# Performance work log

Measured on AMD Instinct MI355X. Metric: run time of the kernel, lower is better.

Reference implementation:

```python
import jax, jax.numpy as jnp
import numpy as np

N = 100000
E = 1_600_000
DIN = 24
DH = 64
DOUT = 12
NEG_SLOPE = 0.01  # torch F.leaky_relu default


def setup_inputs() -> dict:
    key = jax.random.key(0)
    ks = jax.random.split(key, 18)
    inp = {}
    inp["feats"] = jax.random.normal(ks[0], (N, DIN), dtype=jnp.float32)
    inp["e_w"] = jax.random.uniform(ks[1], (E, 1), dtype=jnp.float32)
    inp["snorm_n"] = jnp.ones((N, 1), dtype=jnp.float32)
    inp["snorm_e"] = jnp.ones((E, 1), dtype=jnp.float32)
    inp["src"] = jax.random.randint(ks[2], (E,), 0, N, dtype=jnp.int32)
    inp["dst"] = jax.random.randint(ks[3], (E,), 0, N, dtype=jnp.int32)
    s = 0.05
    inp["emb_h_W"] = jax.random.normal(ks[4], (DH, DIN), dtype=jnp.float32) * s
    inp["emb_h_b"] = jnp.zeros((DH,), dtype=jnp.float32)
    inp["emb_e_W"] = jax.random.normal(ks[5], (DH, 1), dtype=jnp.float32) * s
    inp["emb_e_b"] = jnp.zeros((DH,), dtype=jnp.float32)
    inp["W_self1"] = jax.random.normal(ks[6], (DH, DH), dtype=jnp.float32) * s
    inp["W_func1"] = jax.random.normal(ks[7], (DH, DH), dtype=jnp.float32) * s
    inp["attn1"] = jax.random.normal(ks[8], (3 * DH,), dtype=jnp.float32) * s
    inp["W_self2"] = jax.random.normal(ks[9], (DH, DH), dtype=jnp.float32) * s
    inp["W_func2"] = jax.random.normal(ks[10], (DH, DH), dtype=jnp.float32) * s
    inp["attn2"] = jax.random.normal(ks[11], (3 * DH,), dtype=jnp.float32) * s
    inp["lin1_W"] = jax.random.normal(ks[12], (DOUT, DH), dtype=jnp.float32) * s
    inp["lin1_b"] = jnp.zeros((DOUT,), dtype=jnp.float32)
    return inp


def _gat_layer(h, w_edge, src, dst, W_self, W_func, attn):
    # h: [N, d], w_edge: [E, d] edge embedding, attn: [3d]
    h_s = h @ W_self.T                       # linear_self(h)
    z = h @ W_func.T                         # linear_func(h)
    d = z.shape[-1]
    a_src, a_dst, a_w = attn[:d], attn[d:2 * d], attn[2 * d:]
    # attention score: W_a . [z_src, z_dst, w]  (decomposed to avoid [E,3d] concat)
    s_node_src = z @ a_src                   # [N]
    s_node_dst = z @ a_dst                   # [N]
    e = s_node_src[src] + s_node_dst[dst] + w_edge @ a_w  # [E]
    e = jax.nn.leaky_relu(e, NEG_SLOPE)
    # segment softmax over incoming edges per destination node
    m = jax.ops.segment_max(e, dst, num_segments=h.shape[0])
    ex = jnp.exp(e - m[dst])
    denom = jax.ops.segment_sum(ex, dst, num_segments=h.shape[0])
    alpha = ex / denom[dst]                  # [E]
    msg = alpha[:, None] * z[src]            # [E, d]
    agg = jax.ops.segment_sum(msg, dst, num_segments=h.shape[0])  # [N, d]
    # DGL: nodes with no incoming edges keep their old 'h' (not h_s + agg)
    in_deg = jax.ops.segment_sum(jnp.ones_like(e), dst, num_segments=h.shape[0])
    h_mid = jnp.where((in_deg > 0)[:, None], h_s + agg, h)
    return h + jax.nn.relu(h_mid)            # relu then residual


def reference(feats, e_w, snorm_n, snorm_e, src, dst,
              emb_h_W, emb_h_b, emb_e_W, emb_e_b,
              W_self1, W_func1, attn1, W_self2, W_func2, attn2,
              lin1_W, lin1_b):
    feats = feats.reshape(feats.shape[0], -1)
    h = feats @ emb_h_W.T + emb_h_b          # [N, DH]
    e = e_w @ emb_e_W.T + emb_e_b            # [E, DH]
    h = _gat_layer(h, e, src, dst, W_self1, W_func1, attn1)
    h = _gat_layer(h, e, src, dst, W_self2, W_func2, attn2)
    y = h @ lin1_W.T + lin1_b                # [N, DOUT]
    return y
```

## Files before the change

kernel.cpp:

```cpp
#include <hip/hip_runtime.h>
#include <hip/hip_fp16.h>

#define N_NODES 100000
#define N_EDGES 1600000
#define DIN 24
#define DH 64
#define DOUT 12
#define NEG_SLOPE 0.01f
#define NG 64
#define EPG (N_EDGES / NG)
#define NS 4
#define SLICE_N 32768
#define NTOT (NG * N_NODES)
#define SCAN_BLK 4096
#define LDSW 72

#define NB_HIST (NS * NG)
#define NB_SUMDEG ((N_NODES + 255) / 256)
#define NB_SCAN1N ((N_NODES + SCAN_BLK - 1) / SCAN_BLK)
#define NB_SCAT4 ((N_EDGES / 4 + 1023) / 1024)
#define NB_NODE ((N_NODES + 63) / 64)
#define NB_NODE_T ((NB_NODE + 1) / 2)
#define NB_NME ((NB_NODE + 7) / 8)
#define NB_AGG ((N_NODES + 7) / 8)

#define SM_WEMB 18432
#define SM_BIAS 23552
#define SM_HBUF 23808
#define SM_SIZE 60672

typedef _Float16 half8_t __attribute__((ext_vector_type(8)));
typedef float floatx4 __attribute__((ext_vector_type(4)));

__device__ __forceinline__ void dev_consts(const float* emb_e_W, const float* emb_e_b,
                                           const float* attn1, const float* attn2,
                                           float* consts) {
    int lane = threadIdx.x;
    if (lane >= 64) return;
    float w = emb_e_W[lane], b = emb_e_b[lane];
    float a1 = attn1[2 * DH + lane], a2 = attn2[2 * DH + lane];
    float c11 = w * a1, c01 = b * a1, c12 = w * a2, c02 = b * a2;
    for (int off = 32; off; off >>= 1) {
        c11 += __shfl_down(c11, off);
        c01 += __shfl_down(c01, off);
        c12 += __shfl_down(c12, off);
        c02 += __shfl_down(c02, off);
    }
    if (lane == 0) {
        consts[0] = c11; consts[1] = c01; consts[2] = c12; consts[3] = c02;
    }
}

__device__ __forceinline__ void dev_hist(int bid, char* smem, const int* dst,
                                         unsigned char* deg, unsigned char* rank) {
    unsigned* cnt = (unsigned*)smem;
    int s = bid % NS, c = bid / NS;
    for (int i = threadIdx.x; i < SLICE_N / 4; i += 1024) cnt[i] = 0;
    __syncthreads();
    int nbase = s * SLICE_N;
    int start = c * EPG, end = start + EPG;
    for (int i = start + threadIdx.x; i < end; i += 1024) {
        int local = dst[i] - nbase;
        if ((unsigned)local < SLICE_N) {
            unsigned sh = (unsigned)(local & 3) * 8u;
            unsigned old = atomicAdd(&cnt[local >> 2], 1u << sh);
            rank[i] = (unsigned char)((old >> sh) & 255u);
        }
    }
    __syncthreads();
    int nmax = N_NODES - nbase;
    if (nmax > SLICE_N) nmax = SLICE_N;
    unsigned* dw = (unsigned*)(deg + (size_t)c * N_NODES + nbase);
    for (int l = threadIdx.x; l < (nmax >> 2); l += 1024) dw[l] = cnt[l];
}

__device__ __forceinline__ void dev_scan1(int bid, const int* in, int* out,
                                          int* part, int n) {
    __shared__ int lds[256];
    int t = threadIdx.x;
    int base = bid * SCAN_BLK + t * 16;
    int v[16];
    int s = 0;
#pragma unroll
    for (int i = 0; i < 16; ++i) {
        int idx = base + i;
        v[i] = (idx < n) ? in[idx] : 0;
        s += v[i];
    }
    lds[t] = s;
    __syncthreads();
    for (int off = 1; off < 256; off <<= 1) {
        int y = (t >= off) ? lds[t - off] : 0;
        __syncthreads();
        lds[t] += y;
        __syncthreads();
    }
    int run = lds[t] - s;
#pragma unroll
    for (int i = 0; i < 16; ++i) {
        int idx = base + i;
        if (idx < n) out[idx] = run;
        run += v[i];
    }
    if (t == 255) part[bid] = lds[255];
}

__device__ __forceinline__ void dev_sumdeg(int bid, const unsigned char* degB,
                                           int* degN, unsigned char* chunkOff) {
    int n = bid * 256 + threadIdx.x;
    if (n >= N_NODES) return;
    int run = 0;
    for (int g = 0; g < NG; ++g) {
        size_t idx = (size_t)g * N_NODES + n;
        int v = (int)degB[idx];
        chunkOff[idx] = (unsigned char)run;
        run += v;
    }
    degN[n] = run;
}

__device__ __forceinline__ void dev_scat4(int bid, const int* src, const int* dst,
                                          const float* e_w, const unsigned char* rank,
                                          const int* rowStart,
                                          const unsigned char* chunkOff,
                                          unsigned* csr2) {
    int e4 = (bid * 1024 + threadIdx.x) * 4;
    if (e4 >= N_EDGES) return;
    int g = e4 / EPG;
    const unsigned char* co = chunkOff + (size_t)g * N_NODES;
    int4   d4 = *(const int4*)(dst + e4);
    int4   s4 = *(const int4*)(src + e4);
    float4 w4 = *(const float4*)(e_w + e4);
    unsigned r4 = *(const unsigned*)(rank + e4);
    int b0 = rowStart[d4.x] + (int)co[d4.x];
    int b1 = rowStart[d4.y] + (int)co[d4.y];
    int b2 = rowStart[d4.z] + (int)co[d4.z];
    int b3 = rowStart[d4.w] + (int)co[d4.w];
    unsigned q0 = (unsigned)(w4.x * 32768.f); if (q0 > 32767u) q0 = 32767u;
    unsigned q1 = (unsigned)(w4.y * 32768.f); if (q1 > 32767u) q1 = 32767u;
    unsigned q2 = (unsigned)(w4.z * 32768.f); if (q2 > 32767u) q2 = 32767u;
    unsigned q3 = (unsigned)(w4.w * 32768.f); if (q3 > 32767u) q3 = 32767u;
    csr2[b0 + (r4 & 255u)]         = (unsigned)s4.x | (q0 << 17);
    csr2[b1 + ((r4 >> 8) & 255u)]  = (unsigned)s4.y | (q1 << 17);
    csr2[b2 + ((r4 >> 16) & 255u)] = (unsigned)s4.z | (q2 << 17);
    csr2[b3 + (r4 >> 24)]          = (unsigned)s4.w | (q3 << 17);
}

__device__ __forceinline__ void dev_nodeME(int bid, char* smem,
                                           const float* feats, const float* embW,
                                           const float* embB,
                                           const float* Wself, const float* Wfunc,
                                           const float* attn,
                                           __half* h16, __half* zh, __half* hs16,
                                           float* s_src, float* s_dst) {
    _Float16* lds   = (_Float16*)smem;
    _Float16* wembH = (_Float16*)(smem + SM_WEMB);
    float*    biasS = (float*)(smem + SM_BIAS);
    _Float16* hbufA = (_Float16*)(smem + SM_HBUF);
    int tid = threadIdx.x;
    for (int idx = tid; idx < 2 * 64 * 64; idx += 1024) {
        int mat = idx >> 12, rem = idx & 4095;
        int o = rem >> 6, k = rem & 63;
        float v = mat ? Wfunc[rem] : Wself[rem];
        lds[(mat * 64 + o) * LDSW + k] = (_Float16)v;
    }
    for (int idx = tid; idx < 64 * 32; idx += 1024) {
        int o = idx >> 5, k = idx & 31;
        wembH[o * 40 + k] = (_Float16)((k < DIN) ? embW[o * DIN + k] : 0.f);
    }
    if (tid < 64) biasS[tid] = embB[tid];
    __syncthreads();

    int wave = tid >> 6, lane = tid & 63;
    int vb = wave >> 2, wv = wave & 3;
    int quad = lane >> 4, lm = lane & 15;
    float asv[4], adv[4];
#pragma unroll
    for (int t = 0; t < 4; ++t) {
        asv[t] = attn[t * 16 + lm];
        adv[t] = attn[DH + t * 16 + lm];
    }
    const _Float16* bS = lds;
    const _Float16* bF = lds + 64 * LDSW;
    _Float16* hb = hbufA + wave * (16 * 72);

    for (int tb = bid * 4 + vb; tb < NB_NODE; tb += NB_NME * 4) {
        int n0 = (tb * 4 + wv) * 16;
        if (n0 >= N_NODES) continue;

        half8_t afE;
#pragma unroll
        for (int j = 0; j < 8; ++j) afE[j] = (_Float16)0.f;
        if (quad < 3) {
            const float* f = feats + (size_t)(n0 + lm) * DIN + quad * 8;
            float4 q0 = *(const float4*)(f);
            float4 q1 = *(const float4*)(f + 4);
            afE[0] = (_Float16)q0.x; afE[1] = (_Float16)q0.y;
            afE[2] = (_Float16)q0.z; afE[3] = (_Float16)q0.w;
            afE[4] = (_Float16)q1.x; afE[5] = (_Float16)q1.y;
            afE[6] = (_Float16)q1.z; afE[7] = (_Float16)q1.w;
        }
        floatx4 accE[4];
#pragma unroll
        for (int t = 0; t < 4; ++t) accE[t] = (floatx4)0.f;
#pragma unroll
        for (int t = 0; t < 4; ++t) {
            int o = t * 16 + lm;
            half8_t bE = *(const half8_t*)(wembH + o * 40 + quad * 8);
            accE[t] = __builtin_amdgcn_mfma_f32_16x16x32_f16(afE, bE, accE[t], 0, 0, 0);
        }
#pragma unroll
        for (int t = 0; t < 4; ++t) {
            float bv = biasS[t * 16 + lm];
#pragma unroll
            for (int r = 0; r < 4; ++r) {
                float hv = accE[t][r] + bv;
                int node = n0 + quad * 4 + r;
                h16[(size_t)node * DH + t * 16 + lm] = __float2half(hv);
                hb[(quad * 4 + r) * 72 + t * 16 + lm] = (_Float16)hv;
            }
        }
        half8_t afrag[2];
#pragma unroll
        for (int ks = 0; ks < 2; ++ks)
            afrag[ks] = *(const half8_t*)(hb + lm * 72 + ks * 32 + quad * 8);

        floatx4 accS[4], accF[4];
#pragma unroll
        for (int t = 0; t < 4; ++t) { accS[t] = (floatx4)0.f; accF[t] = (floatx4)0.f; }
#pragma unroll
        for (int t = 0; t < 4; ++t) {
            int o = t * 16 + lm;
#pragma unroll
            for (int ks = 0; ks < 2; ++ks) {
                int hoff = o * LDSW + ks * 32 + quad * 8;
                half8_t b1 = *(const half8_t*)(bS + hoff);
                half8_t b2 = *(const half8_t*)(bF + hoff);
                accS[t] = __builtin_amdgcn_mfma_f32_16x16x32_f16(afrag[ks], b1, accS[t], 0, 0, 0);
                accF[t] = __builtin_amdgcn_mfma_f32_16x16x32_f16(afrag[ks], b2, accF[t], 0, 0, 0);
            }
        }

        float ps[4] = {0.f, 0.f, 0.f, 0.f}, pd[4] = {0.f, 0.f, 0.f, 0.f};
#pragma unroll
        for (int t = 0; t < 4; ++t) {
#pragma unroll
            for (int r = 0; r < 4; ++r) {
                int node = n0 + quad * 4 + r;
                float zv = accF[t][r];
                zh[(size_t)node * DH + t * 16 + lm] = __float2half(zv);
                hs16[(size_t)node * DH + t * 16 + lm] = __float2half(accS[t][r]);
                ps[r] += zv * asv[t];
                pd[r] += zv * adv[t];
            }
        }
#pragma unroll
        for (int r = 0; r < 4; ++r) {
            float p1 = ps[r], p2 = pd[r];
            for (int off = 8; off; off >>= 1) {
                p1 += __shfl_xor(p1, off);
                p2 += __shfl_xor(p2, off);
            }
            if (lm == 0) {
                s_src[n0 + quad * 4 + r] = p1;
                s_dst[n0 + quad * 4 + r] = p2;
            }
        }
    }
}

__device__ __forceinline__ void dev_nodeM(int bid, int stride, const __half* h16,
                                          const float* Wself, const float* Wfunc,
                                          const float* attn,
                                          __half* zh, __half* hs16,
                                          float* s_src, float* s_dst) {
    __shared__ _Float16 lds[2 * 64 * LDSW];
    int tid = threadIdx.x;
    for (int idx = tid; idx < 2 * 64 * 64; idx += 256) {
        int mat = idx >> 12, rem = idx & 4095;
        int o = rem >> 6, k = rem & 63;
        float v = mat ? Wfunc[rem] : Wself[rem];
        lds[(mat * 64 + o) * LDSW + k] = (_Float16)v;
    }
    __syncthreads();

    int wave = tid >> 6, lane = tid & 63;
    int quad = lane >> 4, lm = lane & 15;
    float asv[4], adv[4];
#pragma unroll
    for (int t = 0; t < 4; ++t) {
        asv[t] = attn[t * 16 + lm];
        adv[t] = attn[DH + t * 16 + lm];
    }
    const _Float16* bS = lds;
    const _Float16* bF = lds + 64 * LDSW;

    for (int tb = bid; tb < NB_NODE; tb += stride) {
        int n0 = (tb * 4 + wave) * 16;
        if (n0 >= N_NODES) continue;

        const _Float16* hrow = (const _Float16*)h16 + (size_t)(n0 + lm) * DH;
        half8_t afrag[2];
#pragma unroll
        for (int ks = 0; ks < 2; ++ks)
            afrag[ks] = *(const half8_t*)(hrow + ks * 32 + quad * 8);

        floatx4 accS[4], accF[4];
#pragma unroll
        for (int t = 0; t < 4; ++t) { accS[t] = (floatx4)0.f; accF[t] = (floatx4)0.f; }

#pragma unroll
        for (int t = 0; t < 4; ++t) {
            int o = t * 16 + lm;
#pragma unroll
            for (int ks = 0; ks < 2; ++ks) {
                int hoff = o * LDSW + ks * 32 + quad * 8;
                half8_t b1 = *(const half8_t*)(bS + hoff);
                half8_t b2 = *(const half8_t*)(bF + hoff);
                accS[t] = __builtin_amdgcn_mfma_f32_16x16x32_f16(afrag[ks], b1, accS[t], 0, 0, 0);
                accF[t] = __builtin_amdgcn_mfma_f32_16x16x32_f16(afrag[ks], b2, accF[t], 0, 0, 0);
            }
        }

        float ps[4] = {0.f, 0.f, 0.f, 0.f}, pd[4] = {0.f, 0.f, 0.f, 0.f};
#pragma unroll
        for (int t = 0; t < 4; ++t) {
#pragma unroll
            for (int r = 0; r < 4; ++r) {
                int node = n0 + quad * 4 + r;
                float zv = accF[t][r];
                zh[(size_t)node * DH + t * 16 + lm] = __float2half(zv);
                hs16[(size_t)node * DH + t * 16 + lm] = __float2half(accS[t][r]);
                ps[r] += zv * asv[t];
                pd[r] += zv * adv[t];
            }
        }
#pragma unroll
        for (int r = 0; r < 4; ++r) {
            float p1 = ps[r], p2 = pd[r];
            for (int off = 8; off; off >>= 1) {
                p1 += __shfl_xor(p1, off);
                p2 += __shfl_xor(p2, off);
            }
            if (lm == 0) {
                s_src[n0 + quad * 4 + r] = p1;
                s_dst[n0 + quad * 4 + r] = p2;
            }
        }
    }
}

__global__ void __launch_bounds__(1024, 2)
k_fuse1(const int* __restrict__ dst, unsigned char* __restrict__ deg,
        unsigned char* __restrict__ rank,
        const float* __restrict__ emb_e_W, const float* __restrict__ emb_e_b,
        const float* __restrict__ attn1, const float* __restrict__ attn2,
        float* __restrict__ consts) {
    __shared__ __align__(16) char smem[SLICE_N];
    int bid = blockIdx.x;
    if (bid == 0) { dev_consts(emb_e_W, emb_e_b, attn1, attn2, consts); return; }
    dev_hist(bid - 1, smem, dst, deg, rank);
}

__global__ void k_prep2(const unsigned char* __restrict__ degB, int* __restrict__ degN,
                        unsigned char* __restrict__ chunkOff) {
    dev_sumdeg(blockIdx.x, degB, degN, chunkOff);
}

__global__ void k_prep3(const int* __restrict__ degN, int* __restrict__ row_offN,
                        int* __restrict__ partN) {
    dev_scan1(blockIdx.x, degN, row_offN, partN, N_NODES);
}

__global__ void k_prep4(const int* __restrict__ row_offN, const int* __restrict__ partN,
                        int* __restrict__ rowStart) {
    __shared__ int pfx[32];
    int t = threadIdx.x;
    if (t < 64) {
        int v = (t < NB_SCAN1N) ? partN[t] : 0;
        int x = v;
#pragma unroll
        for (int s = 1; s < 32; s <<= 1) {
            int y = __shfl_up(x, s);
            if (t >= s) x += y;
        }
        if (t < 32) pfx[t] = x - v;
    }
    __syncthreads();
    int n = blockIdx.x * 256 + t;
    if (n < N_NODES) rowStart[n] = row_offN[n] + pfx[n >> 12];
    if (n == 0) rowStart[N_NODES] = N_EDGES;
}

__global__ void __launch_bounds__(1024, 2)
k_fuse5(const float* __restrict__ feats, const float* __restrict__ embW,
        const float* __restrict__ embB,
        __half* __restrict__ h16, const float* __restrict__ Wself1,
        const float* __restrict__ Wfunc1, const float* __restrict__ attn1,
        __half* __restrict__ zh, __half* __restrict__ hs16,
        float* __restrict__ s_src, float* __restrict__ s_dst,
        const int* __restrict__ src, const int* __restrict__ dst,
        const float* __restrict__ e_w, const unsigned char* __restrict__ rank,
        const int* __restrict__ rowStart,
        const unsigned char* __restrict__ chunkOff, unsigned* __restrict__ csr2) {
    __shared__ __align__(16) char smem[SM_SIZE];
    int bid = blockIdx.x;
    if (bid < NB_NME) {
        dev_nodeME(bid, smem, feats, embW, embB, Wself1, Wfunc1, attn1,
                   h16, zh, hs16, s_src, s_dst);
        return;
    }
    dev_scat4(bid - NB_NME, src, dst, e_w, rank, rowStart, chunkOff, csr2);
}

__global__ void __launch_bounds__(256, 4)
k_nodeL(const __half* __restrict__ h16, const float* __restrict__ Wself,
        const float* __restrict__ Wfunc, const float* __restrict__ attn,
        __half* __restrict__ zh, __half* __restrict__ hs16,
        float* __restrict__ s_src, float* __restrict__ s_dst) {
    dev_nodeM(blockIdx.x, NB_NODE_T, h16, Wself, Wfunc, attn, zh, hs16, s_src, s_dst);
}

__global__ void k_agg(const int* __restrict__ rowStart,
                      const unsigned* __restrict__ csr,
                      const float* __restrict__ s_src, const float* __restrict__ s_dstA,
                      const float* __restrict__ consts, int layer,
                      const __half* __restrict__ zh, const __half* __restrict__ hsb,
                      __half* __restrict__ h16,
                      const float* __restrict__ lin_W, const float* __restrict__ lin_b,
                      float* __restrict__ y, int final_layer) {
    int wave = threadIdx.x >> 6, lane = threadIdx.x & 63;
    int half = lane >> 5, hl = lane & 31;
    int eg = (lane >> 3) & 3, c8 = lane & 7;
    int n = blockIdx.x * 8 + wave * 2 + half;
    if (n >= N_NODES) return;
    int rs = rowStart[n];
    int deg = rowStart[n + 1] - rs;
    int degO = __shfl_xor(deg, 32);
    int degmax = deg > degO ? deg : degO;

    float c1 = consts[layer * 2 + 0];
    float c0 = consts[layer * 2 + 1];
    float sd = s_dstA[n];

    float acc[8];
#pragma unroll
    for (int k = 0; k < 8; ++k) acc[k] = 0.f;
    float ssl = 0.f;
    int lbase = lane & 32;

    for (int base = 0; base < degmax; base += 32) {
        float ex = 0.f;
        int s0 = 0;
        int idx = base + hl;
        if (idx < deg) {
            unsigned w = csr[rs + idx];
            s0 = (int)(w & 0x1FFFFu);
            float ew = (float)(w >> 17) * (1.f / 32768.f);
            float e = s_src[s0] + sd + ew * c1 + c0;
            e = (e > 0.f) ? e : NEG_SLOPE * e;
            ex = __expf(e);
        }
        ssl += ex;
        int cnt = degmax - base;
        if (cnt > 32) cnt = 32;
#pragma unroll 4
        for (int jb = 0; jb < cnt; jb += 4) {
            int srcl = lbase + jb + eg;
            int sj = __shfl(s0, srcl);
            float exj = __shfl(ex, srcl);
            unsigned boff = ((unsigned)sj << 7) | ((unsigned)c8 << 4);
            half8_t zv = *(const half8_t*)((const char*)zh + boff);
#pragma unroll
            for (int k = 0; k < 8; ++k) acc[k] += exj * (float)zv[k];
        }
    }
#pragma unroll
    for (int k = 0; k < 8; ++k) {
        acc[k] += __shfl_xor(acc[k], 8);
        acc[k] += __shfl_xor(acc[k], 16);
    }
    ssl += __shfl_xor(ssl, 16); ssl += __shfl_xor(ssl, 8);
    ssl += __shfl_xor(ssl, 4);  ssl += __shfl_xor(ssl, 2);
    ssl += __shfl_xor(ssl, 1);

    unsigned noff = ((unsigned)n << 7) | ((unsigned)c8 << 4);
    half8_t hv8 = *(const half8_t*)((const char*)h16 + noff);
    float hold[8];
#pragma unroll
    for (int k = 0; k < 8; ++k) hold[k] = (float)hv8[k];
    float hnew[8];
    if (deg == 0) {
#pragma unroll
        for (int k = 0; k < 8; ++k) hnew[k] = hold[k] + fmaxf(hold[k], 0.f);
    } else {
        float rinv = 1.f / ssl;
        half8_t hs8 = *(const half8_t*)((const char*)hsb + noff);
#pragma unroll
        for (int k = 0; k < 8; ++k)
            hnew[k] = hold[k] + fmaxf((float)hs8[k] + acc[k] * rinv, 0.f);
    }

    if (!final_layer) {
        if (eg == 0) {
            half8_t o8;
#pragma unroll
            for (int k = 0; k < 8; ++k) o8[k] = (_Float16)hnew[k];
            *(half8_t*)((char*)h16 + noff) = o8;
        }
    } else {
#pragma unroll
        for (int t = 0; t < 3; ++t) {
            int o = eg * 3 + t;
            const float* wr = lin_W + o * DH + c8 * 8;
            float p = 0.f;
#pragma unroll
            for (int k = 0; k < 8; ++k) p += hnew[k] * wr[k];
            p += __shfl_xor(p, 1); p += __shfl_xor(p, 2); p += __shfl_xor(p, 4);
            if (c8 == 0) y[n * DOUT + o] = p + lin_b[o];
        }
    }
}

extern "C" void kernel_launch(void* const* d_in, const int* in_sizes, int n_in,
                              void* d_out, int out_size, void* d_ws, size_t ws_size,
                              hipStream_t stream) {
    const float* feats   = (const float*)d_in[0];
    const float* e_w     = (const float*)d_in[1];
    const int*   src     = (const int*)d_in[4];
    const int*   dst     = (const int*)d_in[5];
    const float* emb_h_W = (const float*)d_in[6];
    const float* emb_h_b = (const float*)d_in[7];
    const float* emb_e_W = (const float*)d_in[8];
    const float* emb_e_b = (const float*)d_in[9];
    const float* Wself[2] = {(const float*)d_in[10], (const float*)d_in[13]};
    const float* Wfunc[2] = {(const float*)d_in[11], (const float*)d_in[14]};
    const float* attn[2]  = {(const float*)d_in[12], (const float*)d_in[15]};
    const float* lin1_W  = (const float*)d_in[16];
    const float* lin1_b  = (const float*)d_in[17];
    float* y = (float*)d_out;

    char* ws = (char*)d_ws;
    size_t off = 0;
    auto alloc = [&](size_t bytes) {
        void* p = ws + off;
        off += (bytes + 255) & ~(size_t)255;
        return p;
    };
    __half*         h16      = (__half*)alloc((size_t)N_NODES * DH * 2);
    __half*         zh       = (__half*)alloc((size_t)N_NODES * DH * 2);
    __half*         hs16     = (__half*)alloc((size_t)N_NODES * DH * 2);
    unsigned*       csr2     = (unsigned*)alloc((size_t)N_EDGES * 4);
    float*          s_src    = (float*)alloc((size_t)N_NODES * 4);
    float*          s_dst    = (float*)alloc((size_t)N_NODES * 4);
    int*            row_offN = (int*)alloc((size_t)(N_NODES + 1) * 4);
    int*            rowStart = (int*)alloc((size_t)(N_NODES + 1) * 4);
    unsigned char*  deg      = (unsigned char*)alloc((size_t)NTOT + 256);
    unsigned char*  chunkOff = (unsigned char*)alloc((size_t)NTOT + 256);
    unsigned char*  rank     = (unsigned char*)alloc((size_t)N_EDGES);
    int*            degN     = (int*)alloc((size_t)N_NODES * 4);
    int*            partN    = (int*)alloc(1024 * 4);
    float*          consts   = (float*)alloc(4 * 4);

    k_fuse1<<<1 + NB_HIST, 1024, 0, stream>>>(dst, deg, rank, emb_e_W, emb_e_b,
                                              attn[0], attn[1], consts);
    k_prep2<<<NB_SUMDEG, 256, 0, stream>>>(deg, degN, chunkOff);
    k_prep3<<<NB_SCAN1N, 256, 0, stream>>>(degN, row_offN, partN);
    k_prep4<<<NB_SUMDEG, 256, 0, stream>>>(row_offN, partN, rowStart);
    k_fuse5<<<NB_NME + NB_SCAT4, 1024, 0, stream>>>(
        feats, emb_h_W, emb_h_b, h16, Wself[0], Wfunc[0], attn[0],
        zh, hs16, s_src, s_dst,
        src, dst, e_w, rank, rowStart, chunkOff, csr2);
    k_agg<<<NB_AGG, 256, 0, stream>>>(rowStart, csr2, s_src, s_dst, consts, 0,
                                      zh, hs16, h16, lin1_W, lin1_b, y, 0);
    k_nodeL<<<NB_NODE_T, 256, 0, stream>>>(h16, Wself[1], Wfunc[1], attn[1],
                                           zh, hs16, s_src, s_dst);
    k_agg<<<NB_AGG, 256, 0, stream>>>(rowStart, csr2, s_src, s_dst, consts, 1,
                                      zh, hs16, h16, lin1_W, lin1_b, y, 1);
}
```

Baseline: 286.7 us.

## Fuse layer-1 aggregation with layer-2 node transform into one kernel

```diff
diff --git a/kernel.cpp b/kernel.cpp
--- a/kernel.cpp
+++ b/kernel.cpp
@@ -20,8 +20,8 @@
 #define NB_SCAN1N ((N_NODES + SCAN_BLK - 1) / SCAN_BLK)
 #define NB_SCAT4 ((N_EDGES / 4 + 1023) / 1024)
 #define NB_NODE ((N_NODES + 63) / 64)
-#define NB_NODE_T ((NB_NODE + 1) / 2)
 #define NB_NME ((NB_NODE + 7) / 8)
+#define NB_AGGG (N_NODES / 16)
 #define NB_AGG ((N_NODES + 7) / 8)
 
 #define SM_WEMB 18432
@@ -269,87 +269,6 @@
     }
 }
 
-__device__ __forceinline__ void dev_nodeM(int bid, int stride, const __half* h16,
-                                          const float* Wself, const float* Wfunc,
-                                          const float* attn,
-                                          __half* zh, __half* hs16,
-                                          float* s_src, float* s_dst) {
-    __shared__ _Float16 lds[2 * 64 * LDSW];
-    int tid = threadIdx.x;
-    for (int idx = tid; idx < 2 * 64 * 64; idx += 256) {
-        int mat = idx >> 12, rem = idx & 4095;
-        int o = rem >> 6, k = rem & 63;
-        float v = mat ? Wfunc[rem] : Wself[rem];
-        lds[(mat * 64 + o) * LDSW + k] = (_Float16)v;
-    }
-    __syncthreads();
-
-    int wave = tid >> 6, lane = tid & 63;
-    int quad = lane >> 4, lm = lane & 15;
-    float asv[4], adv[4];
-#pragma unroll
-    for (int t = 0; t < 4; ++t) {
-        asv[t] = attn[t * 16 + lm];
-        adv[t] = attn[DH + t * 16 + lm];
-    }
-    const _Float16* bS = lds;
-    const _Float16* bF = lds + 64 * LDSW;
-
-    for (int tb = bid; tb < NB_NODE; tb += stride) {
-        int n0 = (tb * 4 + wave) * 16;
-        if (n0 >= N_NODES) continue;
-
-        const _Float16* hrow = (const _Float16*)h16 + (size_t)(n0 + lm) * DH;
-        half8_t afrag[2];
-#pragma unroll
-        for (int ks = 0; ks < 2; ++ks)
-            afrag[ks] = *(const half8_t*)(hrow + ks * 32 + quad * 8);
-
-        floatx4 accS[4], accF[4];
-#pragma unroll
-        for (int t = 0; t < 4; ++t) { accS[t] = (floatx4)0.f; accF[t] = (floatx4)0.f; }
-
-#pragma unroll
-        for (int t = 0; t < 4; ++t) {
-            int o = t * 16 + lm;
-#pragma unroll
-            for (int ks = 0; ks < 2; ++ks) {
-                int hoff = o * LDSW + ks * 32 + quad * 8;
-                half8_t b1 = *(const half8_t*)(bS + hoff);
-                half8_t b2 = *(const half8_t*)(bF + hoff);
-                accS[t] = __builtin_amdgcn_mfma_f32_16x16x32_f16(afrag[ks], b1, accS[t], 0, 0, 0);
-                accF[t] = __builtin_amdgcn_mfma_f32_16x16x32_f16(afrag[ks], b2, accF[t], 0, 0, 0);
-            }
-        }
-
-        float ps[4] = {0.f, 0.f, 0.f, 0.f}, pd[4] = {0.f, 0.f, 0.f, 0.f};
-#pragma unroll
-        for (int t = 0; t < 4; ++t) {
-#pragma unroll
-            for (int r = 0; r < 4; ++r) {
-                int node = n0 + quad * 4 + r;
-                float zv = accF[t][r];
-                zh[(size_t)node * DH + t * 16 + lm] = __float2half(zv);
-                hs16[(size_t)node * DH + t * 16 + lm] = __float2half(accS[t][r]);
-                ps[r] += zv * asv[t];
-                pd[r] += zv * adv[t];
-            }
-        }
-#pragma unroll
-        for (int r = 0; r < 4; ++r) {
-            float p1 = ps[r], p2 = pd[r];
-            for (int off = 8; off; off >>= 1) {
-                p1 += __shfl_xor(p1, off);
-                p2 += __shfl_xor(p2, off);
-            }
-            if (lm == 0) {
-                s_src[n0 + quad * 4 + r] = p1;
-                s_dst[n0 + quad * 4 + r] = p2;
-            }
-        }
-    }
-}
-
 __global__ void __launch_bounds__(1024, 2)
 k_fuse1(const int* __restrict__ dst, unsigned char* __restrict__ deg,
         unsigned char* __restrict__ rank,
@@ -413,12 +332,164 @@
     dev_scat4(bid - NB_NME, src, dst, e_w, rank, rowStart, chunkOff, csr2);
 }
 
-__global__ void __launch_bounds__(256, 4)
-k_nodeL(const __half* __restrict__ h16, const float* __restrict__ Wself,
-        const float* __restrict__ Wfunc, const float* __restrict__ attn,
-        __half* __restrict__ zh, __half* __restrict__ hs16,
-        float* __restrict__ s_src, float* __restrict__ s_dst) {
-    dev_nodeM(blockIdx.x, NB_NODE_T, h16, Wself, Wfunc, attn, zh, hs16, s_src, s_dst);
+__global__ void __launch_bounds__(512, 6)
+k_aggG(const int* __restrict__ rowStart, const unsigned* __restrict__ csr,
+       const float* __restrict__ s_src, const float* __restrict__ s_dstA,
+       const float* __restrict__ consts,
+       const __half* __restrict__ zh, const __half* __restrict__ hsb,
+       __half* __restrict__ h16,
+       const float* __restrict__ Wself, const float* __restrict__ Wfunc,
+       const float* __restrict__ attn,
+       __half* __restrict__ zh2, __half* __restrict__ hs2,
+       float* __restrict__ s_src2, float* __restrict__ s_dst2) {
+    __shared__ _Float16 wlds[2 * 64 * LDSW];
+    __shared__ _Float16 hbuf[16 * 72];
+    int tid = threadIdx.x;
+    for (int idx = tid; idx < 2 * 64 * 64; idx += 512) {
+        int mat = idx >> 12, rem = idx & 4095;
+        int o = rem >> 6, k = rem & 63;
+        float v = mat ? Wfunc[rem] : Wself[rem];
+        wlds[(mat * 64 + o) * LDSW + k] = (_Float16)v;
+    }
+
+    int wave = tid >> 6, lane = tid & 63;
+    int half = lane >> 5, hl = lane & 31;
+    int eg = (lane >> 3) & 3, c8 = lane & 7;
+    int n = blockIdx.x * 16 + wave * 2 + half;
+    int rs = rowStart[n];
+    int deg = rowStart[n + 1] - rs;
+    int degO = __shfl_xor(deg, 32);
+    int degmax = deg > degO ? deg : degO;
+
+    float c1 = consts[0];
+    float c0 = consts[1];
+    float sd = s_dstA[n];
+
+    float acc[8];
+#pragma unroll
+    for (int k = 0; k < 8; ++k) acc[k] = 0.f;
+    float ssl = 0.f;
+    int lbase = lane & 32;
+
+    for (int base = 0; base < degmax; base += 32) {
+        float ex = 0.f;
+        int s0 = 0;
+        int idx = base + hl;
+        if (idx < deg) {
+            unsigned w = csr[rs + idx];
+            s0 = (int)(w & 0x1FFFFu);
+            float ew = (float)(w >> 17) * (1.f / 32768.f);
+            float e = s_src[s0] + sd + ew * c1 + c0;
+            e = (e > 0.f) ? e : NEG_SLOPE * e;
+            ex = __expf(e);
+        }
+        ssl += ex;
+        int cnt = degmax - base;
+        if (cnt > 32) cnt = 32;
+#pragma unroll 4
+        for (int jb = 0; jb < cnt; jb += 4) {
+            int srcl = lbase + jb + eg;
+            int sj = __shfl(s0, srcl);
+            float exj = __shfl(ex, srcl);
+            unsigned boff = ((unsigned)sj << 7) | ((unsigned)c8 << 4);
+            half8_t zv = *(const half8_t*)((const char*)zh + boff);
+#pragma unroll
+            for (int k = 0; k < 8; ++k) acc[k] += exj * (float)zv[k];
+        }
+    }
+#pragma unroll
+    for (int k = 0; k < 8; ++k) {
+        acc[k] += __shfl_xor(acc[k], 8);
+        acc[k] += __shfl_xor(acc[k], 16);
+    }
+    ssl += __shfl_xor(ssl, 16); ssl += __shfl_xor(ssl, 8);
+    ssl += __shfl_xor(ssl, 4);  ssl += __shfl_xor(ssl, 2);
+    ssl += __shfl_xor(ssl, 1);
+
+    unsigned noff = ((unsigned)n << 7) | ((unsigned)c8 << 4);
+    half8_t hv8 = *(const half8_t*)((const char*)h16 + noff);
+    float hold[8];
+#pragma unroll
+    for (int k = 0; k < 8; ++k) hold[k] = (float)hv8[k];
+    float hnew[8];
+    if (deg == 0) {
+#pragma unroll
+        for (int k = 0; k < 8; ++k) hnew[k] = hold[k] + fmaxf(hold[k], 0.f);
+    } else {
+        float rinv = 1.f / ssl;
+        half8_t hs8 = *(const half8_t*)((const char*)hsb + noff);
+#pragma unroll
+        for (int k = 0; k < 8; ++k)
+            hnew[k] = hold[k] + fmaxf((float)hs8[k] + acc[k] * rinv, 0.f);
+    }
+
+    if (eg == 0) {
+        half8_t o8;
+#pragma unroll
+        for (int k = 0; k < 8; ++k) o8[k] = (_Float16)hnew[k];
+        *(half8_t*)((char*)h16 + noff) = o8;
+        *(half8_t*)(hbuf + (wave * 2 + half) * 72 + c8 * 8) = o8;
+    }
+    __syncthreads();
+
+    if (wave == 0) {
+        int quad = lane >> 4, lm = lane & 15;
+        float asv[4], adv[4];
+#pragma unroll
+        for (int t = 0; t < 4; ++t) {
+            asv[t] = attn[t * 16 + lm];
+            adv[t] = attn[DH + t * 16 + lm];
+        }
+        half8_t afrag[2];
+#pragma unroll
+        for (int ks = 0; ks < 2; ++ks)
+            afrag[ks] = *(const half8_t*)(hbuf + lm * 72 + ks * 32 + quad * 8);
+
+        floatx4 accS[4], accF[4];
+#pragma unroll
+        for (int t = 0; t < 4; ++t) { accS[t] = (floatx4)0.f; accF[t] = (floatx4)0.f; }
+        const _Float16* bS = wlds;
+        const _Float16* bF = wlds + 64 * LDSW;
+#pragma unroll
+        for (int t = 0; t < 4; ++t) {
+            int o = t * 16 + lm;
+#pragma unroll
+            for (int ks = 0; ks < 2; ++ks) {
+                int hoff = o * LDSW + ks * 32 + quad * 8;
+                half8_t b1 = *(const half8_t*)(bS + hoff);
+                half8_t b2 = *(const half8_t*)(bF + hoff);
+                accS[t] = __builtin_amdgcn_mfma_f32_16x16x32_f16(afrag[ks], b1, accS[t], 0, 0, 0);
+                accF[t] = __builtin_amdgcn_mfma_f32_16x16x32_f16(afrag[ks], b2, accF[t], 0, 0, 0);
+            }
+        }
+
+        int n0 = blockIdx.x * 16;
+        float ps[4] = {0.f, 0.f, 0.f, 0.f}, pd[4] = {0.f, 0.f, 0.f, 0.f};
+#pragma unroll
+        for (int t = 0; t < 4; ++t) {
+#pragma unroll
+            for (int r = 0; r < 4; ++r) {
+                int node = n0 + quad * 4 + r;
+                float zv = accF[t][r];
+                zh2[(size_t)node * DH + t * 16 + lm] = __float2half(zv);
+                hs2[(size_t)node * DH + t * 16 + lm] = __float2half(accS[t][r]);
+                ps[r] += zv * asv[t];
+                pd[r] += zv * adv[t];
+            }
+        }
+#pragma unroll
+        for (int r = 0; r < 4; ++r) {
+            float p1 = ps[r], p2 = pd[r];
+            for (int off = 8; off; off >>= 1) {
+                p1 += __shfl_xor(p1, off);
+                p2 += __shfl_xor(p2, off);
+            }
+            if (lm == 0) {
+                s_src2[n0 + quad * 4 + r] = p1;
+                s_dst2[n0 + quad * 4 + r] = p2;
+            }
+        }
+    }
 }
 
 __global__ void k_agg(const int* __restrict__ rowStart,
@@ -550,9 +621,13 @@
     __half*         h16      = (__half*)alloc((size_t)N_NODES * DH * 2);
     __half*         zh       = (__half*)alloc((size_t)N_NODES * DH * 2);
     __half*         hs16     = (__half*)alloc((size_t)N_NODES * DH * 2);
+    __half*         zh2      = (__half*)alloc((size_t)N_NODES * DH * 2);
+    __half*         hs2      = (__half*)alloc((size_t)N_NODES * DH * 2);
     unsigned*       csr2     = (unsigned*)alloc((size_t)N_EDGES * 4);
     float*          s_src    = (float*)alloc((size_t)N_NODES * 4);
     float*          s_dst    = (float*)alloc((size_t)N_NODES * 4);
+    float*          s_src2   = (float*)alloc((size_t)N_NODES * 4);
+    float*          s_dst2   = (float*)alloc((size_t)N_NODES * 4);
     int*            row_offN = (int*)alloc((size_t)(N_NODES + 1) * 4);
     int*            rowStart = (int*)alloc((size_t)(N_NODES + 1) * 4);
     unsigned char*  deg      = (unsigned char*)alloc((size_t)NTOT + 256);
@@ -571,10 +646,9 @@
         feats, emb_h_W, emb_h_b, h16, Wself[0], Wfunc[0], attn[0],
         zh, hs16, s_src, s_dst,
         src, dst, e_w, rank, rowStart, chunkOff, csr2);
-    k_agg<<<NB_AGG, 256, 0, stream>>>(rowStart, csr2, s_src, s_dst, consts, 0,
-                                      zh, hs16, h16, lin1_W, lin1_b, y, 0);
-    k_nodeL<<<NB_NODE_T, 256, 0, stream>>>(h16, Wself[1], Wfunc[1], attn[1],
-                                           zh, hs16, s_src, s_dst);
-    k_agg<<<NB_AGG, 256, 0, stream>>>(rowStart, csr2, s_src, s_dst, consts, 1,
-                                      zh, hs16, h16, lin1_W, lin1_b, y, 1);
-}
+    k_aggG<<<NB_AGGG, 512, 0, stream>>>(rowStart, csr2, s_src, s_dst, consts,
+                                        zh, hs16, h16, Wself[1], Wfunc[1], attn[1],
+                                        zh2, hs2, s_src2, s_dst2);
+    k_agg<<<NB_AGG, 256, 0, stream>>>(rowStart, csr2, s_src2, s_dst2, consts, 1,
+                                      zh2, hs2, h16, lin1_W, lin1_b, y, 1);
+}
```

New measurement: 301.2 us. 1.05x slower.
